# Optimization experiments

Measured on AMD Instinct MI355X. Metric: run time of the kernel, lower is better.

The kernel has to match this reference:

```python
import jax, jax.numpy as jnp
import numpy as np
from math import sqrt

B, IN_F, OUT_F = 32, 1024, 4096
DROPOUT_RATE = 0.1


def setup_inputs() -> dict:
    key = jax.random.key(0)
    kx, kw, kb, kmw, kmb = jax.random.split(key, 5)
    k = sqrt(1.0 / IN_F)  # He-style init std from source
    x = jax.random.normal(kx, (B, IN_F), dtype=jnp.float32)
    weight = k * jax.random.normal(kw, (IN_F, OUT_F), dtype=jnp.float32)
    bias = k * jax.random.normal(kb, (OUT_F,), dtype=jnp.float32)
    # per-sample Bernoulli keep masks: rand > dropout_rate (no 1/(1-p) rescale in source)
    w_mask = jax.random.uniform(kmw, (B, IN_F, OUT_F)) > DROPOUT_RATE
    b_mask = jax.random.uniform(kmb, (B, OUT_F)) > DROPOUT_RATE
    return {"x": x, "weight": weight, "bias": bias, "w_mask": w_mask, "b_mask": b_mask}


def reference(x, weight, bias, w_mask, b_mask):
    # 'w' dropout mode: per-sample masked weight matmul, vectorized over batch
    # (replaces the original Python loop of B GEMVs with one batched contraction).
    mw = w_mask.astype(x.dtype)
    y = jnp.einsum("bi,io,bio->bo", x, weight, mw)  # [B, OUT_F]
    return y + bias[None, :] * b_mask.astype(x.dtype)
```

## Files before the change

kernel.cpp:

```cpp
#include <hip/hip_runtime.h>


#define B_DIM 32
#define IN_F 1024
#define OUT_F 4096
#define N_CHUNK 16
#define I_CHUNK (IN_F / N_CHUNK)
#define O_PER_BLK 1024
#define BO (B_DIM * OUT_F)

__global__ __launch_bounds__(256, 4) void masked_gemv_partial(
    const float* __restrict__ x,
    const float* __restrict__ weight,
    const int* __restrict__ w_mask,
    float* __restrict__ partial)
{
    const int bid   = blockIdx.x;
    const int b     = bid >> 6;
    const int s     = bid & 63;
    const int o_blk = s >> 4;
    const int chunk = s & 15;
    const int i0    = chunk * I_CHUNK;
    const int o     = o_blk * O_PER_BLK + (threadIdx.x << 2);

    __shared__ float xs[I_CHUNK];
    if (threadIdx.x < I_CHUNK) xs[threadIdx.x] = x[b * IN_F + i0 + threadIdx.x];
    __syncthreads();

    const int*   mptr = w_mask + (size_t)b * IN_F * OUT_F + (size_t)i0 * OUT_F + o;
    const float* wptr = weight + (size_t)i0 * OUT_F + o;

    float4 acc = {0.f, 0.f, 0.f, 0.f};
#pragma unroll 8
    for (int i = 0; i < I_CHUNK; ++i) {
        const float xi = xs[i];
        const int4   m = *(const int4*)  (mptr + (size_t)i * OUT_F);
        const float4 w = *(const float4*)(wptr + (size_t)i * OUT_F);
        acc.x = fmaf(xi * (float)m.x, w.x, acc.x);
        acc.y = fmaf(xi * (float)m.y, w.y, acc.y);
        acc.z = fmaf(xi * (float)m.z, w.z, acc.z);
        acc.w = fmaf(xi * (float)m.w, w.w, acc.w);
    }

    *(float4*)(partial + (size_t)chunk * BO + b * OUT_F + o) = acc;
}

__global__ __launch_bounds__(256) void reduce_bias_kernel(
    const float* __restrict__ partial,
    const float* __restrict__ bias,
    const int* __restrict__ b_mask,
    float* __restrict__ out)
{
    const int tid = blockIdx.x * 256 + threadIdx.x;
    float s = 0.f;
#pragma unroll
    for (int c = 0; c < N_CHUNK; ++c)
        s += partial[(size_t)c * BO + tid];
    const int o = tid & (OUT_F - 1);
    out[tid] = fmaf(bias[o], (float)b_mask[tid], s);
}

extern "C" void kernel_launch(void* const* d_in, const int* in_sizes, int n_in,
                              void* d_out, int out_size, void* d_ws, size_t ws_size,
                              hipStream_t stream) {
    const float* x      = (const float*)d_in[0];
    const float* weight = (const float*)d_in[1];
    const float* bias   = (const float*)d_in[2];
    const int*   w_mask = (const int*)d_in[3];
    const int*   b_mask = (const int*)d_in[4];
    float* out     = (float*)d_out;
    float* partial = (float*)d_ws;

    masked_gemv_partial<<<B_DIM * 64, 256, 0, stream>>>(x, weight, w_mask, partial);
    reduce_bias_kernel<<<BO / 256, 256, 0, stream>>>(partial, bias, b_mask, out);
}
```

Measured before the change: 702.8 us.

## Cover full output row per block with nontemporal mask loads and select-based masking

Result: no change. 691.2 us (-1.6%).

```diff
diff --git a/kernel.cpp b/kernel.cpp
--- a/kernel.cpp
+++ b/kernel.cpp
@@ -4,45 +4,70 @@
 #define B_DIM 32
 #define IN_F 1024
 #define OUT_F 4096
-#define N_CHUNK 16
-#define I_CHUNK (IN_F / N_CHUNK)
-#define O_PER_BLK 1024
 #define BO (B_DIM * OUT_F)
+#define I_CHUNK 64
+#define N_CHUNK (IN_F / I_CHUNK)
 
-__global__ __launch_bounds__(256, 4) void masked_gemv_partial(
+typedef int   v4i __attribute__((ext_vector_type(4)));
+typedef float v4f __attribute__((ext_vector_type(4)));
+
+__global__ __launch_bounds__(256, 2) void masked_gemv_partial(
     const float* __restrict__ x,
     const float* __restrict__ weight,
     const int* __restrict__ w_mask,
     float* __restrict__ partial)
 {
     const int bid   = blockIdx.x;
-    const int b     = bid >> 6;
-    const int s     = bid & 63;
-    const int o_blk = s >> 4;
-    const int chunk = s & 15;
+    const int b     = bid >> 4;
+    const int chunk = bid & 15;
     const int i0    = chunk * I_CHUNK;
-    const int o     = o_blk * O_PER_BLK + (threadIdx.x << 2);
 
     __shared__ float xs[I_CHUNK];
     if (threadIdx.x < I_CHUNK) xs[threadIdx.x] = x[b * IN_F + i0 + threadIdx.x];
     __syncthreads();
 
-    const int*   mptr = w_mask + (size_t)b * IN_F * OUT_F + (size_t)i0 * OUT_F + o;
-    const float* wptr = weight + (size_t)i0 * OUT_F + o;
+    const int o4 = threadIdx.x << 2;
+    const int* __restrict__ mrow =
+        w_mask + ((size_t)b * IN_F + i0) * OUT_F + o4;
+    const float* __restrict__ wrow = weight + (size_t)i0 * OUT_F + o4;
 
-    float4 acc = {0.f, 0.f, 0.f, 0.f};
-#pragma unroll 8
+    v4f acc0 = {0,0,0,0}, acc1 = {0,0,0,0}, acc2 = {0,0,0,0}, acc3 = {0,0,0,0};
+
+#pragma unroll 2
     for (int i = 0; i < I_CHUNK; ++i) {
         const float xi = xs[i];
-        const int4   m = *(const int4*)  (mptr + (size_t)i * OUT_F);
-        const float4 w = *(const float4*)(wptr + (size_t)i * OUT_F);
-        acc.x = fmaf(xi * (float)m.x, w.x, acc.x);
-        acc.y = fmaf(xi * (float)m.y, w.y, acc.y);
-        acc.z = fmaf(xi * (float)m.z, w.z, acc.z);
-        acc.w = fmaf(xi * (float)m.w, w.w, acc.w);
+        const size_t r = (size_t)i * OUT_F;
+        const v4i m0 = __builtin_nontemporal_load((const v4i*)(mrow + r));
+        const v4i m1 = __builtin_nontemporal_load((const v4i*)(mrow + r + 1024));
+        const v4i m2 = __builtin_nontemporal_load((const v4i*)(mrow + r + 2048));
+        const v4i m3 = __builtin_nontemporal_load((const v4i*)(mrow + r + 3072));
+        const v4f w0 = *(const v4f*)(wrow + r);
+        const v4f w1 = *(const v4f*)(wrow + r + 1024);
+        const v4f w2 = *(const v4f*)(wrow + r + 2048);
+        const v4f w3 = *(const v4f*)(wrow + r + 3072);
+        acc0.x = fmaf(m0.x ? xi : 0.f, w0.x, acc0.x);
+        acc0.y = fmaf(m0.y ? xi : 0.f, w0.y, acc0.y);
+        acc0.z = fmaf(m0.z ? xi : 0.f, w0.z, acc0.z);
+        acc0.w = fmaf(m0.w ? xi : 0.f, w0.w, acc0.w);
+        acc1.x = fmaf(m1.x ? xi : 0.f, w1.x, acc1.x);
+        acc1.y = fmaf(m1.y ? xi : 0.f, w1.y, acc1.y);
+        acc1.z = fmaf(m1.z ? xi : 0.f, w1.z, acc1.z);
+        acc1.w = fmaf(m1.w ? xi : 0.f, w1.w, acc1.w);
+        acc2.x = fmaf(m2.x ? xi : 0.f, w2.x, acc2.x);
+        acc2.y = fmaf(m2.y ? xi : 0.f, w2.y, acc2.y);
+        acc2.z = fmaf(m2.z ? xi : 0.f, w2.z, acc2.z);
+        acc2.w = fmaf(m2.w ? xi : 0.f, w2.w, acc2.w);
+        acc3.x = fmaf(m3.x ? xi : 0.f, w3.x, acc3.x);
+        acc3.y = fmaf(m3.y ? xi : 0.f, w3.y, acc3.y);
+        acc3.z = fmaf(m3.z ? xi : 0.f, w3.z, acc3.z);
+        acc3.w = fmaf(m3.w ? xi : 0.f, w3.w, acc3.w);
     }
 
-    *(float4*)(partial + (size_t)chunk * BO + b * OUT_F + o) = acc;
+    float* prow = partial + ((size_t)chunk * B_DIM + b) * OUT_F + o4;
+    __builtin_nontemporal_store(acc0, (v4f*)(prow));
+    __builtin_nontemporal_store(acc1, (v4f*)(prow + 1024));
+    __builtin_nontemporal_store(acc2, (v4f*)(prow + 2048));
+    __builtin_nontemporal_store(acc3, (v4f*)(prow + 3072));
 }
 
 __global__ __launch_bounds__(256) void reduce_bias_kernel(
@@ -71,6 +96,6 @@
     float* out     = (float*)d_out;
     float* partial = (float*)d_ws;
 
-    masked_gemv_partial<<<B_DIM * 64, 256, 0, stream>>>(x, weight, w_mask, partial);
+    masked_gemv_partial<<<B_DIM * N_CHUNK, 256, 0, stream>>>(x, weight, w_mask, partial);
     reduce_bias_kernel<<<BO / 256, 256, 0, stream>>>(partial, bias, b_mask, out);
 }
```
